# Performance work log

Measured on AMD Instinct MI355X. Metric: run time of the kernel, lower is better.

## Reference

```python
import jax, jax.numpy as jnp
import numpy as np

N = 100_000      # total nodes in batched graph
E = 1_600_000    # directed edges (avg degree 16)
G = 64           # graphs in batch
F_IN = 64        # num_features
H = 64           # hl1
GF = 32          # num_global_feats
GH = 32          # global_hl1 (hard-coded in module)


def setup_inputs() -> dict:
    key = jax.random.key(0)
    ks = jax.random.split(key, 24)
    s = 0.1  # weight scale
    inp = {
        "x": jax.random.normal(ks[0], (N, F_IN), jnp.float32),
        "global_feats": jax.random.normal(ks[1], (G * GF,), jnp.float32),
        "conv0_w": jax.random.normal(ks[2], (F_IN, H), jnp.float32) * s,
        "conv0_b": jax.random.normal(ks[3], (H,), jnp.float32) * s,
        "conv1_w": jax.random.normal(ks[4], (H, H), jnp.float32) * s,
        "conv1_b": jax.random.normal(ks[5], (H,), jnp.float32) * s,
        "conv2_w": jax.random.normal(ks[6], (H, H), jnp.float32) * s,
        "conv2_b": jax.random.normal(ks[7], (H,), jnp.float32) * s,
        "lin1_w": jax.random.normal(ks[8], (H, H), jnp.float32) * s,
        "lin1_b": jax.random.normal(ks[9], (H,), jnp.float32) * s,
        "glob_w": jax.random.normal(ks[10], (GF, GH), jnp.float32) * s,
        "glob_b": jax.random.normal(ks[11], (GH,), jnp.float32) * s,
        "lin2_w": jax.random.normal(ks[12], (H + GH, H), jnp.float32) * s,
        "lin2_b": jax.random.normal(ks[13], (H,), jnp.float32) * s,
        "lin3_w": jax.random.normal(ks[14], (H, H), jnp.float32) * s,
        "lin3_b": jax.random.normal(ks[15], (H,), jnp.float32) * s,
        "lin4_w": jax.random.normal(ks[16], (H, 1), jnp.float32) * s,
        "lin4_b": jax.random.normal(ks[17], (1,), jnp.float32) * s,
        "edge_index": jax.random.randint(ks[18], (2, E), 0, N, jnp.int64) if jax.config.jax_enable_x64 else jax.random.randint(ks[18], (2, E), 0, N, jnp.int32),
        "node_graph_ids": jnp.sort(jax.random.randint(ks[19], (N,), 0, G, jnp.int32)),
    }
    return inp


def reference(x, global_feats, conv0_w, conv0_b, conv1_w, conv1_b, conv2_w, conv2_b,
              lin1_w, lin1_b, glob_w, glob_b, lin2_w, lin2_b, lin3_w, lin3_b,
              lin4_w, lin4_b, edge_index, node_graph_ids):
    # --- GCN symmetric normalization with self-loops (PyG GCNConv default) ---
    loops = jnp.arange(N, dtype=edge_index.dtype)
    src = jnp.concatenate([edge_index[0], loops])  # [E+N]
    dst = jnp.concatenate([edge_index[1], loops])
    deg = jax.ops.segment_sum(jnp.ones_like(dst, jnp.float32), dst, num_segments=N)
    dis = jax.lax.rsqrt(deg)  # deg >= 1 thanks to self-loops
    norm = (dis[src] * dis[dst])[:, None]  # [E+N, 1]

    def gcn_conv(h, W, b):
        h = h @ W                                    # [N, H]
        msg = h[src] * norm                          # gather + scale  [E+N, H]
        return jax.ops.segment_sum(msg, dst, num_segments=N) + b  # scatter-add

    h = jax.nn.relu(gcn_conv(x, conv0_w, conv0_b))
    h = jax.nn.relu(gcn_conv(h, conv1_w, conv1_b))
    h = jax.nn.relu(gcn_conv(h, conv2_w, conv2_b))

    # --- per-graph sum pooling (contiguous slices == segment_sum on sorted ids) ---
    pooled = jax.ops.segment_sum(h, node_graph_ids, num_segments=G)  # [G, H]

    gx = jax.nn.relu(global_feats.reshape(G, GF) @ glob_w + glob_b)  # [G, GH]

    z = jax.nn.relu(pooled @ lin1_w + lin1_b)
    z = jnp.concatenate([z, gx], axis=1)             # [G, H+GH]
    z = jax.nn.relu(z @ lin2_w + lin2_b)
    z = jax.nn.relu(z @ lin3_w + lin3_b)
    out = (z @ lin4_w + lin4_b).squeeze(1)           # [G]
    return out
```

## Files before the change

### kernel.cpp

```cpp
#include <hip/hip_runtime.h>
#include <hip/hip_bf16.h>

#define NTHREADS 256
#define CAP 6144
#define P1_EDGES 8192

typedef unsigned int uint32;

__device__ __forceinline__ void fma8(float4& A0, float4& A1, uint4 v, float w) {
    A0.x += __uint_as_float(v.x << 16) * w;
    A0.y += __uint_as_float(v.x & 0xffff0000u) * w;
    A0.z += __uint_as_float(v.y << 16) * w;
    A0.w += __uint_as_float(v.y & 0xffff0000u) * w;
    A1.x += __uint_as_float(v.z << 16) * w;
    A1.y += __uint_as_float(v.z & 0xffff0000u) * w;
    A1.z += __uint_as_float(v.w << 16) * w;
    A1.w += __uint_as_float(v.w & 0xffff0000u) * w;
}
__device__ __forceinline__ void acc8(float4& A0, float4& A1, uint4 v) {
    A0.x += __uint_as_float(v.x << 16);
    A0.y += __uint_as_float(v.x & 0xffff0000u);
    A0.z += __uint_as_float(v.y << 16);
    A0.w += __uint_as_float(v.y & 0xffff0000u);
    A1.x += __uint_as_float(v.z << 16);
    A1.y += __uint_as_float(v.z & 0xffff0000u);
    A1.z += __uint_as_float(v.w << 16);
    A1.w += __uint_as_float(v.w & 0xffff0000u);
}

__device__ __forceinline__ void stage_W(const float* __restrict__ W, float* sW) {
    int t = threadIdx.x;
    const float4* W4 = (const float4*)W;
    float4* sW4 = (float4*)sW;
#pragma unroll
    for (int i = 0; i < 4; i++) sW4[t + NTHREADS * i] = W4[t + NTHREADS * i];
}

__device__ __forceinline__ void gemm_compute(
    const float* __restrict__ sW, const float* __restrict__ sX,
    const float* __restrict__ sD, __hip_bfloat16* __restrict__ out,
    int n_rows, int row_base) {
    int t = threadIdx.x;
    int c = t & 63;
    int r0 = t >> 6;
    float acc[16];
#pragma unroll
    for (int j = 0; j < 16; j++) acc[j] = 0.f;

    for (int k = 0; k < 64; k += 4) {
        float w0 = sW[(k + 0) * 64 + c];
        float w1 = sW[(k + 1) * 64 + c];
        float w2 = sW[(k + 2) * 64 + c];
        float w3 = sW[(k + 3) * 64 + c];
#pragma unroll
        for (int j = 0; j < 16; j++) {
            float4 xv = *(const float4*)(sX + (r0 + 4 * j) * 64 + k);
            acc[j] += xv.x * w0 + xv.y * w1 + xv.z * w2 + xv.w * w3;
        }
    }

#pragma unroll
    for (int j = 0; j < 16; j++) {
        int r = row_base + r0 + 4 * j;
        if (r < n_rows) {
            float s = sD ? sD[r0 + 4 * j] : 1.0f;
            out[(size_t)r * 64 + c] = __float2bfloat16(s * acc[j]);
        }
    }
}

__global__ __launch_bounds__(NTHREADS) void pass1_gemm0(
    const int* __restrict__ ei, int nE, int* gcur, uint32* __restrict__ pbuf, int npart,
    const float* __restrict__ x, __hip_bfloat16* __restrict__ U,
    const float* __restrict__ W, int n_rows, int nP1) {
    __shared__ __align__(16) float sW[64 * 64];
    __shared__ __align__(16) float sX[64 * 64];

    int bid = blockIdx.x;
    int t = threadIdx.x;

    if (bid < nP1) {
        int* hist = (int*)sW;
        int* base = hist + npart;
        int* cnt  = base + npart;
        for (int i = t; i < npart; i += NTHREADS) { hist[i] = 0; cnt[i] = 0; }
        __syncthreads();

        int e0 = bid * P1_EDGES;
#pragma unroll 4
        for (int j = 0; j < P1_EDGES / NTHREADS; j++) {
            int e = e0 + j * NTHREADS + t;
            if (e < nE) atomicAdd(&hist[ei[nE + e] >> 8], 1);
        }
        __syncthreads();
        for (int i = t; i < npart; i += NTHREADS) {
            base[i] = hist[i] ? atomicAdd(&gcur[i * 16], hist[i]) : 0;
        }
        __syncthreads();
#pragma unroll 4
        for (int j = 0; j < P1_EDGES / NTHREADS; j++) {
            int e = e0 + j * NTHREADS + t;
            if (e < nE) {
                int s = ei[e];
                int d = ei[nE + e];
                int p = d >> 8;
                int off = atomicAdd(&cnt[p], 1);
                int pos = base[p] + off;
                if (pos < CAP) pbuf[(size_t)p * CAP + pos] = ((uint32)s << 8) | (uint32)(d & 255);
            }
        }
        return;
    }

    int row_base = (bid - nP1) * 64;
    stage_W(W, sW);
    float4* sX4 = (float4*)sX;
#pragma unroll
    for (int i = 0; i < 4; i++) {
        int idx = t + NTHREADS * i;
        int r = row_base + (idx >> 4);
        float4 v = make_float4(0.f, 0.f, 0.f, 0.f);
        if (r < n_rows) v = ((const float4*)(x + (size_t)r * 64))[idx & 15];
        sX4[idx] = v;
    }
    __syncthreads();
    gemm_compute(sW, sX, nullptr, U, n_rows, row_base);
}

__global__ __launch_bounds__(512) void scanP(const int* __restrict__ gcur, int* pbase,
                                             int npart, int n, int nE, int* row_ptr) {
    __shared__ int sm[512];
    int t = threadIdx.x;
    int v = (t < npart) ? gcur[t * 16] : 0;
    sm[t] = v;
    __syncthreads();
    for (int off = 1; off < 512; off <<= 1) {
        int a = (t >= off) ? sm[t - off] : 0;
        __syncthreads();
        sm[t] += a;
        __syncthreads();
    }
    if (t < npart) pbase[t] = sm[t] - v;
    if (t == 0) row_ptr[n] = nE;
}

__global__ __launch_bounds__(NTHREADS) void pass2(
    const uint32* __restrict__ pbuf, const int* __restrict__ gcur,
    const int* __restrict__ pbase, int* __restrict__ row_ptr,
    float* __restrict__ dis, int* __restrict__ col, int n) {
    __shared__ int hist[256];
    __shared__ int excl[256];
    __shared__ int cnt[256];
    __shared__ int sm[256];

    int p = blockIdx.x;
    int t = threadIdx.x;
    hist[t] = 0;
    cnt[t] = 0;
    __syncthreads();

    int total = gcur[p * 16];
    if (total > CAP) total = CAP;
    const uint32* pb = pbuf + (size_t)p * CAP;

    for (int i = t; i < total; i += NTHREADS) atomicAdd(&hist[pb[i] & 255], 1);
    __syncthreads();

    sm[t] = hist[t];
    __syncthreads();
    for (int off = 1; off < 256; off <<= 1) {
        int a = (t >= off) ? sm[t - off] : 0;
        __syncthreads();
        sm[t] += a;
        __syncthreads();
    }
    excl[t] = sm[t] - hist[t];
    __syncthreads();

    int rbase = pbase[p];
    int node = p * 256 + t;
    if (node < n) {
        row_ptr[node] = rbase + excl[t];
        dis[node] = rsqrtf(1.0f + (float)hist[t]);
    }

    for (int i = t; i < total; i += NTHREADS) {
        uint32 v = pb[i];
        int dl = v & 255;
        int off = atomicAdd(&cnt[dl], 1);
        col[rbase + excl[dl] + off] = (int)(v >> 8);
    }
}

template <bool WEIGHTED>
__device__ __forceinline__ void gather_row(
    const uint4* __restrict__ T8, const float* __restrict__ dis,
    const float* __restrict__ bias,
    const int* __restrict__ row_ptr, const int* __restrict__ col,
    int node, int q, float* __restrict__ sXrow, int n) {
    float4 o0, o1;
    if (node < n) {
        float dn = dis[node];
        float4 a0 = make_float4(0.f, 0.f, 0.f, 0.f);
        float4 a1 = make_float4(0.f, 0.f, 0.f, 0.f);
        {
            uint4 sv = T8[(size_t)node * 8 + q];
            if (WEIGHTED) fma8(a0, a1, sv, dn);
            else          acc8(a0, a1, sv);
        }
        int e0 = row_ptr[node];
        int e1 = row_ptr[node + 1];
        int e = e0;
        for (; e + 7 < e1; e += 8) {
            int s0 = col[e],     s1 = col[e + 1], s2 = col[e + 2], s3 = col[e + 3];
            int s4 = col[e + 4], s5 = col[e + 5], s6 = col[e + 6], s7 = col[e + 7];
            uint4 v0 = T8[(size_t)s0 * 8 + q];
            uint4 v1 = T8[(size_t)s1 * 8 + q];
            uint4 v2 = T8[(size_t)s2 * 8 + q];
            uint4 v3 = T8[(size_t)s3 * 8 + q];
            uint4 v4 = T8[(size_t)s4 * 8 + q];
            uint4 v5 = T8[(size_t)s5 * 8 + q];
            uint4 v6 = T8[(size_t)s6 * 8 + q];
            uint4 v7 = T8[(size_t)s7 * 8 + q];
            if (WEIGHTED) {
                fma8(a0, a1, v0, dis[s0]); fma8(a0, a1, v1, dis[s1]);
                fma8(a0, a1, v2, dis[s2]); fma8(a0, a1, v3, dis[s3]);
                fma8(a0, a1, v4, dis[s4]); fma8(a0, a1, v5, dis[s5]);
                fma8(a0, a1, v6, dis[s6]); fma8(a0, a1, v7, dis[s7]);
            } else {
                acc8(a0, a1, v0); acc8(a0, a1, v1); acc8(a0, a1, v2); acc8(a0, a1, v3);
                acc8(a0, a1, v4); acc8(a0, a1, v5); acc8(a0, a1, v6); acc8(a0, a1, v7);
            }
        }
        for (; e + 3 < e1; e += 4) {
            int s0 = col[e], s1 = col[e + 1], s2 = col[e + 2], s3 = col[e + 3];
            uint4 v0 = T8[(size_t)s0 * 8 + q];
            uint4 v1 = T8[(size_t)s1 * 8 + q];
            uint4 v2 = T8[(size_t)s2 * 8 + q];
            uint4 v3 = T8[(size_t)s3 * 8 + q];
            if (WEIGHTED) {
                fma8(a0, a1, v0, dis[s0]); fma8(a0, a1, v1, dis[s1]);
                fma8(a0, a1, v2, dis[s2]); fma8(a0, a1, v3, dis[s3]);
            } else {
                acc8(a0, a1, v0); acc8(a0, a1, v1); acc8(a0, a1, v2); acc8(a0, a1, v3);
            }
        }
        for (; e < e1; e++) {
            int s0 = col[e];
            uint4 v0 = T8[(size_t)s0 * 8 + q];
            if (WEIGHTED) fma8(a0, a1, v0, dis[s0]);
            else          acc8(a0, a1, v0);
        }
        float4 b0 = ((const float4*)bias)[q * 2];
        float4 b1 = ((const float4*)bias)[q * 2 + 1];
        o0.x = fmaxf(b0.x + dn * a0.x, 0.f);
        o0.y = fmaxf(b0.y + dn * a0.y, 0.f);
        o0.z = fmaxf(b0.z + dn * a0.z, 0.f);
        o0.w = fmaxf(b0.w + dn * a0.w, 0.f);
        o1.x = fmaxf(b1.x + dn * a1.x, 0.f);
        o1.y = fmaxf(b1.y + dn * a1.y, 0.f);
        o1.z = fmaxf(b1.z + dn * a1.z, 0.f);
        o1.w = fmaxf(b1.w + dn * a1.w, 0.f);
    } else {
        o0 = make_float4(0.f, 0.f, 0.f, 0.f);
        o1 = o0;
    }
    ((float4*)sXrow)[q * 2] = o0;
    ((float4*)sXrow)[q * 2 + 1] = o1;
}

template <bool WEIGHTED>
__global__ __launch_bounds__(NTHREADS) void agg_gemm(
    const __hip_bfloat16* __restrict__ Tin, __hip_bfloat16* __restrict__ Tout,
    const float* __restrict__ W, const float* __restrict__ dis,
    const float* __restrict__ bias,
    const int* __restrict__ row_ptr, const int* __restrict__ col, int n) {
    __shared__ __align__(16) float sW[64 * 64];
    __shared__ __align__(16) float sX[64 * 64];
    __shared__ float sD[64];
    int t = threadIdx.x;
    int row_base = blockIdx.x * 64;

    stage_W(W, sW);
    if (t < 64) {
        int r = row_base + t;
        sD[t] = (r < n) ? dis[r] : 0.f;
    }

    const uint4* T8 = (const uint4*)Tin;
    int q = t & 7;
    int l = t >> 3;
    gather_row<WEIGHTED>(T8, dis, bias, row_ptr, col, row_base + l,      q, sX + l * 64,        n);
    gather_row<WEIGHTED>(T8, dis, bias, row_ptr, col, row_base + 32 + l, q, sX + (32 + l) * 64, n);
    __syncthreads();

    gemm_compute(sW, sX, sD, Tout, n, row_base);
}

__global__ __launch_bounds__(NTHREADS) void agg_pool(
    const __hip_bfloat16* __restrict__ Tin,
    const float* __restrict__ dis, const float* __restrict__ bias,
    const int* __restrict__ row_ptr, const int* __restrict__ col,
    const int* __restrict__ gid, float* __restrict__ pooled, int n) {
    __shared__ __align__(16) float sX[64 * 64];
    __shared__ int sG[64];
    int t = threadIdx.x;
    int row_base = blockIdx.x * 64;

    if (t < 64) {
        int r = row_base + t;
        sG[t] = (r < n) ? gid[r] : -1;
    }

    const uint4* T8 = (const uint4*)Tin;
    int q = t & 7;
    int l = t >> 3;
    gather_row<false>(T8, dis, bias, row_ptr, col, row_base + l,      q, sX + l * 64,        n);
    gather_row<false>(T8, dis, bias, row_ptr, col, row_base + 32 + l, q, sX + (32 + l) * 64, n);
    __syncthreads();

    int f = t & 63;
    int w = t >> 6;
    float racc = 0.f;
    int cur = -1;
#pragma unroll
    for (int i = 0; i < 16; i++) {
        int r = i * 4 + w;
        int g = sG[r];
        if (g != cur) {
            if (cur >= 0 && racc != 0.f) atomicAdd(&pooled[cur * 64 + f], racc);
            racc = 0.f;
            cur = g;
        }
        if (g >= 0) racc += sX[r * 64 + f];
    }
    if (cur >= 0 && racc != 0.f) atomicAdd(&pooled[cur * 64 + f], racc);
}

__global__ __launch_bounds__(NTHREADS) void head_kernel(
    const float* __restrict__ pooled, const float* __restrict__ gf,
    const float* __restrict__ glob_w, const float* __restrict__ glob_b,
    const float* __restrict__ lin1_w, const float* __restrict__ lin1_b,
    const float* __restrict__ lin2_w, const float* __restrict__ lin2_b,
    const float* __restrict__ lin3_w, const float* __restrict__ lin3_b,
    const float* __restrict__ lin4_w, const float* __restrict__ lin4_b,
    float* __restrict__ out) {
    __shared__ float gx[64 * 32];
    __shared__ float zA[64 * 64];
    __shared__ float zB[64 * 64];
    int t = threadIdx.x;

    for (int i = t; i < 64 * 32; i += NTHREADS) {
        int g = i >> 5, j = i & 31;
        float acc = glob_b[j];
        for (int k = 0; k < 32; k++) acc += gf[g * 32 + k] * glob_w[k * 32 + j];
        gx[i] = fmaxf(acc, 0.f);
    }
    for (int i = t; i < 4096; i += NTHREADS) {
        int g = i >> 6, j = i & 63;
        float acc = lin1_b[j];
        for (int k = 0; k < 64; k++) acc += pooled[g * 64 + k] * lin1_w[k * 64 + j];
        zA[i] = fmaxf(acc, 0.f);
    }
    __syncthreads();
    for (int i = t; i < 4096; i += NTHREADS) {
        int g = i >> 6, j = i & 63;
        float acc = lin2_b[j];
        for (int k = 0; k < 64; k++) acc += zA[g * 64 + k] * lin2_w[k * 64 + j];
        for (int k = 0; k < 32; k++) acc += gx[g * 32 + k] * lin2_w[(64 + k) * 64 + j];
        zB[i] = fmaxf(acc, 0.f);
    }
    __syncthreads();
    for (int i = t; i < 4096; i += NTHREADS) {
        int g = i >> 6, j = i & 63;
        float acc = lin3_b[j];
        for (int k = 0; k < 64; k++) acc += zB[g * 64 + k] * lin3_w[k * 64 + j];
        zA[i] = fmaxf(acc, 0.f);
    }
    __syncthreads();
    if (t < 64) {
        float acc = lin4_b[0];
        for (int k = 0; k < 64; k++) acc += zA[t * 64 + k] * lin4_w[k];
        out[t] = acc;
    }
}

extern "C" void kernel_launch(void* const* d_in, const int* in_sizes, int n_in,
                              void* d_out, int out_size, void* d_ws, size_t ws_size,
                              hipStream_t stream) {
    const float* x      = (const float*)d_in[0];
    const float* gf     = (const float*)d_in[1];
    const float* conv_w[3] = {(const float*)d_in[2], (const float*)d_in[4], (const float*)d_in[6]};
    const float* conv_b[3] = {(const float*)d_in[3], (const float*)d_in[5], (const float*)d_in[7]};
    const float* lin1_w = (const float*)d_in[8];
    const float* lin1_b = (const float*)d_in[9];
    const float* glob_w = (const float*)d_in[10];
    const float* glob_b = (const float*)d_in[11];
    const float* lin2_w = (const float*)d_in[12];
    const float* lin2_b = (const float*)d_in[13];
    const float* lin3_w = (const float*)d_in[14];
    const float* lin3_b = (const float*)d_in[15];
    const float* lin4_w = (const float*)d_in[16];
    const float* lin4_b = (const float*)d_in[17];
    const int* ei  = (const int*)d_in[18];
    const int* gid = (const int*)d_in[19];

    const int N = in_sizes[0] / 64;
    const int E = in_sizes[18] / 2;
    const int NPART = (N + 255) >> 8;

    char* ws = (char*)d_ws;
    float* dis     = (float*)ws;                 ws += (size_t)N * 4;
    float* pooled  = (float*)ws;                 ws += 4096 * 4;
    __hip_bfloat16* U  = (__hip_bfloat16*)ws;    ws += (size_t)N * 64 * 2;
    __hip_bfloat16* T1 = (__hip_bfloat16*)ws;    ws += (size_t)N * 64 * 2;
    int*   row_ptr = (int*)ws;                   ws += ((size_t)N + 4) * 4;
    int*   col     = (int*)ws;                   ws += (size_t)E * 4;
    uint32* pbuf   = (uint32*)ws;                ws += (size_t)NPART * CAP * 4;
    int*   gcur    = (int*)ws;                   ws += (size_t)NPART * 16 * 4;
    int*   pbase   = (int*)ws;                   ws += (size_t)((NPART + 15) & ~15) * 4;

    const int nP1 = (E + P1_EDGES - 1) / P1_EDGES;
    const int gemm_blocks = (N + 63) / 64;

    hipMemsetAsync(gcur, 0, (size_t)NPART * 16 * 4, stream);
    hipMemsetAsync(pooled, 0, 4096 * 4, stream);
    pass1_gemm0<<<nP1 + gemm_blocks, NTHREADS, 0, stream>>>(
        ei, E, gcur, pbuf, NPART, x, U, conv_w[0], N, nP1);

    scanP<<<1, 512, 0, stream>>>(gcur, pbase, NPART, N, E, row_ptr);
    pass2<<<NPART, NTHREADS, 0, stream>>>(pbuf, gcur, pbase, row_ptr, dis, col, N);

    agg_gemm<true><<<gemm_blocks, NTHREADS, 0, stream>>>(
        U, T1, conv_w[1], dis, conv_b[0], row_ptr, col, N);

    agg_gemm<false><<<gemm_blocks, NTHREADS, 0, stream>>>(
        T1, U, conv_w[2], dis, conv_b[1], row_ptr, col, N);

    agg_pool<<<gemm_blocks, NTHREADS, 0, stream>>>(
        U, dis, conv_b[2], row_ptr, col, gid, pooled, N);

    head_kernel<<<1, NTHREADS, 0, stream>>>(pooled, gf,
                                            glob_w, glob_b, lin1_w, lin1_b,
                                            lin2_w, lin2_b, lin3_w, lin3_b,
                                            lin4_w, lin4_b, (float*)d_out);
}
```

Baseline: 251.3 us.

## Sort nodes by degree to balance gather work across blocks

Builds a degree-descending permutation of nodes via a counting sort (local histograms in pass2, a scan kernel, and a permutation kernel). The aggregation and pooling kernels then process nodes in permuted order, so rows handled together have similar degrees, which reduces wavefront divergence and load imbalance. The cost is two extra launches, an indirection on every node index, scattered output writes, and loss of locality in graph-id runs for pooling (more atomics).

```diff
diff --git a/kernel.cpp b/kernel.cpp
--- a/kernel.cpp
+++ b/kernel.cpp
@@ -38,8 +38,8 @@
 
 __device__ __forceinline__ void gemm_compute(
     const float* __restrict__ sW, const float* __restrict__ sX,
-    const float* __restrict__ sD, __hip_bfloat16* __restrict__ out,
-    int n_rows, int row_base) {
+    const float* __restrict__ sD, const int* __restrict__ sP,
+    __hip_bfloat16* __restrict__ out, int n_rows, int row_base) {
     int t = threadIdx.x;
     int c = t & 63;
     int r0 = t >> 6;
@@ -61,10 +61,12 @@
 
 #pragma unroll
     for (int j = 0; j < 16; j++) {
-        int r = row_base + r0 + 4 * j;
+        int rr = r0 + 4 * j;
+        int r = row_base + rr;
         if (r < n_rows) {
-            float s = sD ? sD[r0 + 4 * j] : 1.0f;
-            out[(size_t)r * 64 + c] = __float2bfloat16(s * acc[j]);
+            float s = sD ? sD[rr] : 1.0f;
+            int nd = sP ? sP[rr] : r;
+            out[(size_t)nd * 64 + c] = __float2bfloat16(s * acc[j]);
         }
     }
 }
@@ -124,7 +126,7 @@
         sX4[idx] = v;
     }
     __syncthreads();
-    gemm_compute(sW, sX, nullptr, U, n_rows, row_base);
+    gemm_compute(sW, sX, nullptr, nullptr, U, n_rows, row_base);
 }
 
 __global__ __launch_bounds__(512) void scanP(const int* __restrict__ gcur, int* pbase,
@@ -147,16 +149,19 @@
 __global__ __launch_bounds__(NTHREADS) void pass2(
     const uint32* __restrict__ pbuf, const int* __restrict__ gcur,
     const int* __restrict__ pbase, int* __restrict__ row_ptr,
-    float* __restrict__ dis, int* __restrict__ col, int n) {
+    float* __restrict__ dis, int* __restrict__ col,
+    int* __restrict__ keyarr, int* __restrict__ dhist_g, int n) {
     __shared__ int hist[256];
     __shared__ int excl[256];
     __shared__ int cnt[256];
     __shared__ int sm[256];
+    __shared__ int ldh[256];
 
     int p = blockIdx.x;
     int t = threadIdx.x;
     hist[t] = 0;
     cnt[t] = 0;
+    ldh[t] = 0;
     __syncthreads();
 
     int total = gcur[p * 16];
@@ -180,9 +185,15 @@
     int rbase = pbase[p];
     int node = p * 256 + t;
     if (node < n) {
+        int deg = hist[t];
         row_ptr[node] = rbase + excl[t];
-        dis[node] = rsqrtf(1.0f + (float)hist[t]);
-    }
+        dis[node] = rsqrtf(1.0f + (float)deg);
+        int key = 255 - (deg > 255 ? 255 : deg);
+        keyarr[node] = key;
+        atomicAdd(&ldh[key], 1);
+    }
+    __syncthreads();
+    if (ldh[t]) atomicAdd(&dhist_g[t], ldh[t]);
 
     for (int i = t; i < total; i += NTHREADS) {
         uint32 v = pb[i];
@@ -192,14 +203,50 @@
     }
 }
 
+__global__ __launch_bounds__(256) void scanK(int* dhist) {
+    __shared__ int sm[256];
+    int t = threadIdx.x;
+    int v = dhist[t];
+    sm[t] = v;
+    __syncthreads();
+    for (int off = 1; off < 256; off <<= 1) {
+        int a = (t >= off) ? sm[t - off] : 0;
+        __syncthreads();
+        sm[t] += a;
+        __syncthreads();
+    }
+    dhist[t] = sm[t] - v;
+}
+
+__global__ __launch_bounds__(256) void permK(const int* __restrict__ keyarr,
+                                             int* dcur, int* __restrict__ perm, int n) {
+    __shared__ int lh[256];
+    __shared__ int lbase[256];
+    __shared__ int lcnt[256];
+    int t = threadIdx.x;
+    lh[t] = 0;
+    lcnt[t] = 0;
+    __syncthreads();
+    int i = blockIdx.x * 256 + t;
+    int key = (i < n) ? keyarr[i] : -1;
+    if (key >= 0) atomicAdd(&lh[key], 1);
+    __syncthreads();
+    if (lh[t]) lbase[t] = atomicAdd(&dcur[t], lh[t]);
+    __syncthreads();
+    if (key >= 0) {
+        int off = atomicAdd(&lcnt[key], 1);
+        perm[lbase[key] + off] = i;
+    }
+}
+
 template <bool WEIGHTED>
 __device__ __forceinline__ void gather_row(
     const uint4* __restrict__ T8, const float* __restrict__ dis,
     const float* __restrict__ bias,
     const int* __restrict__ row_ptr, const int* __restrict__ col,
-    int node, int q, float* __restrict__ sXrow, int n) {
+    int node, int q, float* __restrict__ sXrow) {
     float4 o0, o1;
-    if (node < n) {
+    if (node >= 0) {
         float dn = dis[node];
         float4 a0 = make_float4(0.f, 0.f, 0.f, 0.f);
         float4 a1 = make_float4(0.f, 0.f, 0.f, 0.f);
@@ -274,49 +321,63 @@
     const __hip_bfloat16* __restrict__ Tin, __hip_bfloat16* __restrict__ Tout,
     const float* __restrict__ W, const float* __restrict__ dis,
     const float* __restrict__ bias,
-    const int* __restrict__ row_ptr, const int* __restrict__ col, int n) {
+    const int* __restrict__ row_ptr, const int* __restrict__ col,
+    const int* __restrict__ perm, int n) {
     __shared__ __align__(16) float sW[64 * 64];
     __shared__ __align__(16) float sX[64 * 64];
     __shared__ float sD[64];
+    __shared__ int sP[64];
     int t = threadIdx.x;
     int row_base = blockIdx.x * 64;
 
     stage_W(W, sW);
     if (t < 64) {
-        int r = row_base + t;
-        sD[t] = (r < n) ? dis[r] : 0.f;
+        int idx = row_base + t;
+        int nd = (idx < n) ? perm[idx] : -1;
+        sP[t] = nd;
+        sD[t] = (nd >= 0) ? dis[nd] : 0.f;
     }
 
     const uint4* T8 = (const uint4*)Tin;
     int q = t & 7;
     int l = t >> 3;
-    gather_row<WEIGHTED>(T8, dis, bias, row_ptr, col, row_base + l,      q, sX + l * 64,        n);
-    gather_row<WEIGHTED>(T8, dis, bias, row_ptr, col, row_base + 32 + l, q, sX + (32 + l) * 64, n);
-    __syncthreads();
-
-    gemm_compute(sW, sX, sD, Tout, n, row_base);
+    int i1 = row_base + l;
+    int i2 = row_base + 32 + l;
+    int nd1 = (i1 < n) ? perm[i1] : -1;
+    int nd2 = (i2 < n) ? perm[i2] : -1;
+    gather_row<WEIGHTED>(T8, dis, bias, row_ptr, col, nd1, q, sX + l * 64);
+    gather_row<WEIGHTED>(T8, dis, bias, row_ptr, col, nd2, q, sX + (32 + l) * 64);
+    __syncthreads();
+
+    gemm_compute(sW, sX, sD, sP, Tout, n, row_base);
 }
 
 __global__ __launch_bounds__(NTHREADS) void agg_pool(
     const __hip_bfloat16* __restrict__ Tin,
     const float* __restrict__ dis, const float* __restrict__ bias,
     const int* __restrict__ row_ptr, const int* __restrict__ col,
-    const int* __restrict__ gid, float* __restrict__ pooled, int n) {
+    const int* __restrict__ gid, const int* __restrict__ perm,
+    float* __restrict__ pooled, int n) {
     __shared__ __align__(16) float sX[64 * 64];
     __shared__ int sG[64];
     int t = threadIdx.x;
     int row_base = blockIdx.x * 64;
 
     if (t < 64) {
-        int r = row_base + t;
-        sG[t] = (r < n) ? gid[r] : -1;
+        int idx = row_base + t;
+        int nd = (idx < n) ? perm[idx] : -1;
+        sG[t] = (nd >= 0) ? gid[nd] : -1;
     }
 
     const uint4* T8 = (const uint4*)Tin;
     int q = t & 7;
     int l = t >> 3;
-    gather_row<false>(T8, dis, bias, row_ptr, col, row_base + l,      q, sX + l * 64,        n);
-    gather_row<false>(T8, dis, bias, row_ptr, col, row_base + 32 + l, q, sX + (32 + l) * 64, n);
+    int i1 = row_base + l;
+    int i2 = row_base + 32 + l;
+    int nd1 = (i1 < n) ? perm[i1] : -1;
+    int nd2 = (i2 < n) ? perm[i2] : -1;
+    gather_row<false>(T8, dis, bias, row_ptr, col, nd1, q, sX + l * 64);
+    gather_row<false>(T8, dis, bias, row_ptr, col, nd2, q, sX + (32 + l) * 64);
     __syncthreads();
 
     int f = t & 63;
@@ -419,26 +480,35 @@
     uint32* pbuf   = (uint32*)ws;                ws += (size_t)NPART * CAP * 4;
     int*   gcur    = (int*)ws;                   ws += (size_t)NPART * 16 * 4;
     int*   pbase   = (int*)ws;                   ws += (size_t)((NPART + 15) & ~15) * 4;
+    int*   keyarr  = (int*)ws;                   ws += (size_t)N * 4;
+    int*   dhist   = (int*)ws;                   ws += 256 * 4;
+    int*   perm    = (int*)ws;                   ws += (size_t)N * 4;
 
     const int nP1 = (E + P1_EDGES - 1) / P1_EDGES;
     const int gemm_blocks = (N + 63) / 64;
+    const int nb_N = (N + 255) / 256;
 
     hipMemsetAsync(gcur, 0, (size_t)NPART * 16 * 4, stream);
     hipMemsetAsync(pooled, 0, 4096 * 4, stream);
+    hipMemsetAsync(dhist, 0, 256 * 4, stream);
     pass1_gemm0<<<nP1 + gemm_blocks, NTHREADS, 0, stream>>>(
         ei, E, gcur, pbuf, NPART, x, U, conv_w[0], N, nP1);
 
     scanP<<<1, 512, 0, stream>>>(gcur, pbase, NPART, N, E, row_ptr);
-    pass2<<<NPART, NTHREADS, 0, stream>>>(pbuf, gcur, pbase, row_ptr, dis, col, N);
+    pass2<<<NPART, NTHREADS, 0, stream>>>(pbuf, gcur, pbase, row_ptr, dis, col,
+                                          keyarr, dhist, N);
+
+    scanK<<<1, 256, 0, stream>>>(dhist);
+    permK<<<nb_N, 256, 0, stream>>>(keyarr, dhist, perm, N);
 
     agg_gemm<true><<<gemm_blocks, NTHREADS, 0, stream>>>(
-        U, T1, conv_w[1], dis, conv_b[0], row_ptr, col, N);
+        U, T1, conv_w[1], dis, conv_b[0], row_ptr, col, perm, N);
 
     agg_gemm<false><<<gemm_blocks, NTHREADS, 0, stream>>>(
-        T1, U, conv_w[2], dis, conv_b[1], row_ptr, col, N);
+        T1, U, conv_w[2], dis, conv_b[1], row_ptr, col, perm, N);
 
     agg_pool<<<gemm_blocks, NTHREADS, 0, stream>>>(
-        U, dis, conv_b[2], row_ptr, col, gid, pooled, N);
+        U, dis, conv_b[2], row_ptr, col, gid, perm, pooled, N);
 
     head_kernel<<<1, NTHREADS, 0, stream>>>(pooled, gf,
                                             glob_w, glob_b, lin1_w, lin1_b,
```

After: 262.9 us. 4.6% more time.
